# Kernel optimization log

Hardware: AMD Instinct MI355X
Metric: run time of the kernel (lower is better)

Reference implementation:

```python
import jax, jax.numpy as jnp
import numpy as np

NUM_HEADS = 4
EPS = 1e-12  # torch F.normalize eps


def conv1x1(x, w):
    # x: (b,c,h,w), w: (co,ci,1,1) -> pointwise conv == channel GEMM
    return jnp.einsum('bchw,dc->bdhw', x, w[:, :, 0, 0])


def dwconv3x3(x, w):
    # depthwise 3x3, groups = channels; w: (c,1,3,3)
    c = x.shape[1]
    return jax.lax.conv_general_dilated(
        x, w, window_strides=(1, 1), padding=((1, 1), (1, 1)),
        dimension_numbers=('NCHW', 'OIHW', 'NCHW'), feature_group_count=c)


def l2_normalize(x, axis=-1):
    n = jnp.sqrt(jnp.sum(x * x, axis=axis, keepdims=True))
    return x / jnp.maximum(n, EPS)


def setup_inputs() -> dict:
    key = jax.random.key(0)
    ks = jax.random.split(key, 8)
    b, c, h, w = 4, 192, 128, 128
    s = 0.05
    return {
        'x': jax.random.normal(ks[0], (b, c, h, w), jnp.float32),
        'wq': jax.random.normal(ks[1], (c, c, 1, 1), jnp.float32) * s,
        'wq_dw': jax.random.normal(ks[2], (c, 1, 3, 3), jnp.float32) * s,
        'wk': jax.random.normal(ks[3], (c, c, 1, 1), jnp.float32) * s,
        'wk_dw': jax.random.normal(ks[4], (c, 1, 3, 3), jnp.float32) * s,
        'wv': jax.random.normal(ks[5], (c, c, 1, 1), jnp.float32) * s,
        'wv_dw': jax.random.normal(ks[6], (c, 1, 3, 3), jnp.float32) * s,
        'temperature': jnp.ones((NUM_HEADS, 1, 1), jnp.float32),
    }


def reference(x, wq, wq_dw, wk, wk_dw, wv, wv_dw, temperature):
    b, c, h, w = x.shape
    hd = NUM_HEADS
    ch = c // hd  # per-head channels
    n = h * w

    q = dwconv3x3(conv1x1(x, wq), wq_dw)
    k = dwconv3x3(conv1x1(x, wk), wk_dw)
    v = dwconv3x3(conv1x1(x, wv), wv_dw)

    # b (head c) h w -> b head c (h w)
    q = q.reshape(b, hd, ch, n)
    k = k.reshape(b, hd, ch, n)
    v = v.reshape(b, hd, ch, n)

    q = l2_normalize(q, axis=-1)
    k = l2_normalize(k, axis=-1)

    # channel-wise attention: (c x N) @ (N x c) -> (c x c)
    attn = jnp.einsum('bhcn,bhdn->bhcd', q, k) * temperature  # temperature: (head,1,1)
    attn = jax.nn.softmax(attn, axis=-1)
    out = jnp.einsum('bhcd,bhdn->bhcn', attn, v)
    return out.reshape(b, c, h, w)
```

## Files before the change

kernel.cpp:

```cpp
#include <hip/hip_runtime.h>
#include <hip/hip_bf16.h>


typedef __attribute__((ext_vector_type(8))) short short8;
typedef __attribute__((ext_vector_type(4))) float f32x4;

#define NB 4
#define NC 192
#define NN 16384
#define CH 48
#define NWELEM 115780
#define NZERO 38400
#define LDP 200

__device__ inline unsigned short f2bf(float f) {
  union { float f; unsigned int u; } c; c.f = f;
  unsigned int r = c.u + 0x7FFF + ((c.u >> 16) & 1);
  return (unsigned short)(r >> 16);
}
__device__ inline float bf2f(unsigned short u) {
  union { unsigned int u; float f; } c; c.u = ((unsigned int)u) << 16;
  return c.f;
}

__device__ inline bool detect_f32(const unsigned short* x) {
  int l = threadIdx.x & 63;
  unsigned short u = x[2 * (l * 997 + 1)];
  int e = (u >> 7) & 0xFF;
  bool extreme = (e < 90) || (e > 165);
  return __popcll(__ballot(extreme)) >= 8;
}

__global__ __launch_bounds__(256) void k_pre(const unsigned short* __restrict__ x,
                                             const void* wq, const void* wk, const void* wv,
                                             const void* wqd, const void* wkd, const void* wvd,
                                             const void* temp,
                                             unsigned short* __restrict__ canon,
                                             float* __restrict__ zbase) {
  int blk = blockIdx.x;
  if (blk >= 453) {
    int i = (blk - 453) * 256 + threadIdx.x;
    if (i < NZERO) zbase[i] = 0.f;
    return;
  }
  bool f32 = detect_f32(x);
  int i = blk * 256 + threadIdx.x;
  if (i >= NWELEM) return;
  const void* src; int off;
  if (i < 36864)       { src = wq;  off = i; }
  else if (i < 73728)  { src = wk;  off = i - 36864; }
  else if (i < 110592) { src = wv;  off = i - 73728; }
  else if (i < 112320) { src = wqd; off = i - 110592; }
  else if (i < 114048) { src = wkd; off = i - 112320; }
  else if (i < 115776) { src = wvd; off = i - 114048; }
  else                 { src = temp; off = i - 115776; }
  canon[i] = f32 ? f2bf(((const float*)src)[off])
                 : ((const unsigned short*)src)[off];
}

__global__ __launch_bounds__(256) void k_conv(const unsigned short* __restrict__ Wall,
                                              const unsigned short* __restrict__ X,
                                              unsigned short* __restrict__ Yall) {
  __shared__ __align__(16) unsigned short Xs[128 * LDP];
  bool f32 = detect_f32(X);
  int b = blockIdx.y, p0 = blockIdx.x * 128;
  int tid = threadIdx.x;
  if (f32) {
    const float* Xf = (const float*)X + (size_t)b * NC * NN + p0;
    for (int it = 0; it < 12; ++it) {
      int idx = it * 256 + tid;
      int c = (idx >> 5) * 2, pq = idx & 31;
      float4 v0 = *(const float4*)(Xf + (size_t)c * NN + pq * 4);
      float4 v1 = *(const float4*)(Xf + (size_t)(c + 1) * NN + pq * 4);
#pragma unroll
      for (int j = 0; j < 4; ++j) {
        unsigned int u = ((unsigned int)f2bf((&v1.x)[j]) << 16) | f2bf((&v0.x)[j]);
        *(unsigned int*)(&Xs[(pq * 4 + j) * LDP + c]) = u;
      }
    }
  } else {
    const unsigned short* Xb = X + (size_t)b * NC * NN + p0;
    for (int it = 0; it < 12; ++it) {
      int idx = it * 256 + tid;
      int c = (idx >> 5) * 2, pq = idx & 31;
      ushort4 v0 = *(const ushort4*)(Xb + (size_t)c * NN + pq * 4);
      ushort4 v1 = *(const ushort4*)(Xb + (size_t)(c + 1) * NN + pq * 4);
#pragma unroll
      for (int j = 0; j < 4; ++j) {
        unsigned int u = ((unsigned int)((&v1.x)[j]) << 16) | (unsigned int)((&v0.x)[j]);
        *(unsigned int*)(&Xs[(pq * 4 + j) * LDP + c]) = u;
      }
    }
  }
  __syncthreads();
  int lane = tid & 63, w = tid >> 6;
  int wm = w & 1, wn = w >> 1;
  int lrow = lane & 15, lq = lane >> 4;
  short8 bf[6][4];
#pragma unroll
  for (int ks = 0; ks < 6; ++ks)
    for (int nt = 0; nt < 4; ++nt)
      bf[ks][nt] = *(const short8*)(&Xs[(wn * 64 + nt * 16 + lrow) * LDP + ks * 32 + lq * 8]);
  for (int dt = 0; dt < 9; ++dt) {
    int d0 = dt * 64;
    f32x4 acc[2][4];
    for (int mt = 0; mt < 2; ++mt)
      for (int nt = 0; nt < 4; ++nt) acc[mt][nt] = (f32x4){0.f, 0.f, 0.f, 0.f};
    for (int ks = 0; ks < 6; ++ks) {
      int k = ks * 32 + lq * 8;
      short8 a[2];
      for (int mt = 0; mt < 2; ++mt)
        a[mt] = *(const short8*)(Wall + (size_t)(d0 + wm * 32 + mt * 16 + lrow) * NC + k);
      for (int mt = 0; mt < 2; ++mt)
        for (int nt = 0; nt < 4; ++nt)
          acc[mt][nt] = __builtin_amdgcn_mfma_f32_16x16x32_bf16(a[mt], bf[ks][nt], acc[mt][nt], 0, 0, 0);
    }
    int proj = dt / 3, c0 = (dt % 3) * 64;
    unsigned short* Yb = Yall + (((size_t)proj * NB + b) * NC) * NN;
    for (int mt = 0; mt < 2; ++mt)
      for (int nt = 0; nt < 4; ++nt)
        for (int r = 0; r < 4; ++r) {
          int c = c0 + wm * 32 + mt * 16 + lq * 4 + r;
          int p = p0 + wn * 64 + nt * 16 + lrow;
          Yb[(size_t)c * NN + p] = f2bf(acc[mt][nt][r]);
        }
  }
}

__device__ inline void cvtrow(short8 raw, unsigned short lo, unsigned short hi,
                              float* dst) {
  dst[0] = bf2f(lo);
#pragma unroll
  for (int j = 0; j < 8; ++j) dst[j + 1] = bf2f((unsigned short)raw[j]);
  dst[9] = bf2f(hi);
}

__global__ __launch_bounds__(256) void k_dwconv(const unsigned short* __restrict__ Yall,
                                                const unsigned short* __restrict__ Wdall,
                                                unsigned short* __restrict__ Pq,
                                                unsigned short* __restrict__ Pk,
                                                unsigned short* __restrict__ Pv,
                                                float* __restrict__ ssq,
                                                float* __restrict__ ssk) {
  int y = blockIdx.x, b = blockIdx.y;
  int proj = y / NC, c = y % NC;
  int tid = threadIdx.x;
  int lane = tid & 63, ch = tid & 15, rg = tid >> 4;
  const unsigned short* base = Yall + (((size_t)proj * NB + b) * NC + c) * NN;
  unsigned short* P = (proj == 0 ? Pq : (proj == 1 ? Pk : Pv));
  float* ss = (proj == 0 ? ssq : (proj == 1 ? ssk : nullptr));
  int r0 = rg * 8;

  short8 raw[10];
  unsigned short hl[10], hr[10];
#pragma unroll
  for (int i = 0; i < 10; ++i) {
    int gy = r0 - 1 + i;
    const unsigned short* rp = base + gy * 128 + ch * 8;
    if (gy >= 0 && gy < 128) {
      raw[i] = *(const short8*)rp;
      hl[i] = (ch > 0)  ? rp[-1] : (unsigned short)0;
      hr[i] = (ch < 15) ? rp[8]  : (unsigned short)0;
    } else {
      raw[i] = (short8){0, 0, 0, 0, 0, 0, 0, 0};
      hl[i] = 0;
      hr[i] = 0;
    }
  }

  float wk9[9];
#pragma unroll
  for (int i = 0; i < 9; ++i) wk9[i] = bf2f(Wdall[(proj * NC + c) * 9 + i]);

  float rows[3][10];
  cvtrow(raw[0], hl[0], hr[0], rows[0]);
  cvtrow(raw[1], hl[1], hr[1], rows[1]);
  float ssacc = 0.f;
#pragma unroll
  for (int r = 0; r < 8; ++r) {
    cvtrow(raw[r + 2], hl[r + 2], hr[r + 2], rows[(r + 2) % 3]);
    float z[8];
#pragma unroll
    for (int j = 0; j < 8; ++j) z[j] = 0.f;
#pragma unroll
    for (int dy = 0; dy < 3; ++dy) {
      const float* f = rows[(r + dy) % 3];
      float w0 = wk9[dy * 3], w1 = wk9[dy * 3 + 1], w2 = wk9[dy * 3 + 2];
#pragma unroll
      for (int j = 0; j < 8; ++j) z[j] += w0 * f[j] + w1 * f[j + 1] + w2 * f[j + 2];
    }
    short8 sv;
#pragma unroll
    for (int j = 0; j < 8; ++j) { sv[j] = (short)f2bf(z[j]); ssacc += z[j] * z[j]; }
    *(short8*)(P + ((size_t)b * NC + c) * NN + (r0 + r) * 128 + ch * 8) = sv;
  }
  if (ss) {
    for (int off = 32; off; off >>= 1) ssacc += __shfl_down(ssacc, off);
    if (lane == 0) atomicAdd(&ss[b * NC + c], ssacc);
  }
}

__global__ __launch_bounds__(256) void k_attn(const unsigned short* __restrict__ Qp,
                                              const unsigned short* __restrict__ Kp,
                                              float* __restrict__ S) {
  __shared__ float Sred[CH * CH];
  int bh = blockIdx.y, chunk = blockIdx.x;
  int b = bh >> 2, h = bh & 3;
  int tid = threadIdx.x, lane = tid & 63, w = tid >> 6;
  int lrow = lane & 15, lq = lane >> 4;
  const unsigned short* Qb = Qp + ((size_t)b * NC + h * CH) * NN;
  const unsigned short* Kb = Kp + ((size_t)b * NC + h * CH) * NN;
  int nbase = chunk * 1024 + w * 256;
  f32x4 acc[3][3];
  for (int i = 0; i < 3; ++i)
    for (int j = 0; j < 3; ++j) acc[i][j] = (f32x4){0.f, 0.f, 0.f, 0.f};
  for (int ks = 0; ks < 8; ++ks) {
    int n = nbase + ks * 32 + lq * 8;
    short8 a[3], bb[3];
    for (int t = 0; t < 3; ++t) a[t]  = *(const short8*)(Qb + (size_t)(t * 16 + lrow) * NN + n);
    for (int t = 0; t < 3; ++t) bb[t] = *(const short8*)(Kb + (size_t)(t * 16 + lrow) * NN + n);
    for (int ti = 0; ti < 3; ++ti)
      for (int tj = 0; tj < 3; ++tj)
        acc[ti][tj] = __builtin_amdgcn_mfma_f32_16x16x32_bf16(a[ti], bb[tj], acc[ti][tj], 0, 0, 0);
  }
  for (int i = tid; i < CH * CH; i += 256) Sred[i] = 0.f;
  __syncthreads();
  for (int ti = 0; ti < 3; ++ti)
    for (int tj = 0; tj < 3; ++tj)
      for (int r = 0; r < 4; ++r) {
        int row = ti * 16 + lq * 4 + r, col = tj * 16 + lrow;
        atomicAdd(&Sred[row * CH + col], acc[ti][tj][r]);
      }
  __syncthreads();
  float* Sg = S + bh * (CH * CH);
  for (int i = tid; i < CH * CH; i += 256) atomicAdd(&Sg[i], Sred[i]);
}

__global__ void k_softmax(const float* __restrict__ S, const float* __restrict__ ssq,
                          const float* __restrict__ ssk, const unsigned short* __restrict__ tempc,
                          float* __restrict__ AT) {
  int bh = blockIdx.x, b = bh >> 2, h = bh & 3;
  int i = threadIdx.x;
  if (i >= CH) return;
  float t = bf2f(tempc[h]);
  float rq = 1.f / fmaxf(sqrtf(ssq[b * NC + h * CH + i]), 1e-12f);
  const float* Srow = S + bh * (CH * CH) + i * CH;
  float l[CH];
  float m = -1e30f;
  for (int j = 0; j < CH; ++j) {
    float rk = 1.f / fmaxf(sqrtf(ssk[b * NC + h * CH + j]), 1e-12f);
    l[j] = Srow[j] * rq * rk * t;
    m = fmaxf(m, l[j]);
  }
  float s = 0.f;
  for (int j = 0; j < CH; ++j) { l[j] = __expf(l[j] - m); s += l[j]; }
  float inv = 1.f / s;
  for (int j = 0; j < CH; ++j) AT[bh * (CH * CH) + j * CH + i] = l[j] * inv;
}

__global__ __launch_bounds__(256) void k_out(const float* __restrict__ AT,
                                             const unsigned short* __restrict__ Vp,
                                             void* __restrict__ Out,
                                             const unsigned short* __restrict__ x) {
  bool f32 = detect_f32(x);
  int bh = blockIdx.y, b = bh >> 2, h = bh & 3;
  int p0 = (blockIdx.x * 256 + threadIdx.x) * 2;
  const float* A = AT + bh * (CH * CH);
  const unsigned short* Vb = Vp + ((size_t)b * NC + h * CH) * NN;
  float a1[CH], a2[CH];
  for (int i = 0; i < CH; ++i) { a1[i] = 0.f; a2[i] = 0.f; }
  for (int j = 0; j < CH; ++j) {
    unsigned int u = *(const unsigned int*)(Vb + (size_t)j * NN + p0);
    float v1 = bf2f((unsigned short)(u & 0xFFFF));
    float v2 = bf2f((unsigned short)(u >> 16));
    const float* Aj = A + j * CH;
    for (int i = 0; i < CH; ++i) {
      float a = Aj[i];
      a1[i] += a * v1;
      a2[i] += a * v2;
    }
  }
  size_t obase = ((size_t)b * NC + h * CH) * NN;
  if (f32) {
    float* Of = (float*)Out;
    for (int i = 0; i < CH; ++i)
      *(float2*)(Of + obase + (size_t)i * NN + p0) = make_float2(a1[i], a2[i]);
  } else {
    unsigned short* Ob = (unsigned short*)Out;
    for (int i = 0; i < CH; ++i) {
      unsigned int u = ((unsigned int)f2bf(a2[i]) << 16) | f2bf(a1[i]);
      *(unsigned int*)(Ob + obase + (size_t)i * NN + p0) = u;
    }
  }
}

extern "C" void kernel_launch(void* const* d_in, const int* in_sizes, int n_in,
                              void* d_out, int out_size, void* d_ws, size_t ws_size,
                              hipStream_t stream) {
  const unsigned short* x = (const unsigned short*)d_in[0];

  const size_t TEN = (size_t)NB * NC * NN;
  unsigned short* bufA = (unsigned short*)d_ws;
  unsigned short* bufB = bufA + TEN;
  unsigned short* bufV = bufB + TEN;
  unsigned short* Yall = bufV + TEN;
  float* ssq = (float*)(Yall + 3 * TEN);
  float* ssk = ssq + NB * NC;
  float* S   = ssk + NB * NC;
  float* AT  = S + 16 * CH * CH;
  unsigned short* canon = (unsigned short*)(AT + 16 * CH * CH);
  const unsigned short* Wall = canon;
  const unsigned short* Wdall = canon + 110592;
  const unsigned short* Tmp = canon + 115776;

  k_pre<<<453 + (NZERO + 255) / 256, 256, 0, stream>>>(
      x, d_in[1], d_in[3], d_in[5], d_in[2], d_in[4], d_in[6], d_in[7], canon, ssq);
  k_conv<<<dim3(NN / 128, NB), 256, 0, stream>>>(Wall, x, Yall);
  k_dwconv<<<dim3(3 * NC, NB), 256, 0, stream>>>(Yall, Wdall, bufA, bufB, bufV, ssq, ssk);
  k_attn<<<dim3(16, 16), 256, 0, stream>>>(bufA, bufB, S);
  k_softmax<<<16, 64, 0, stream>>>(S, ssq, ssk, Tmp, AT);
  k_out<<<dim3(NN / 512, 16), 256, 0, stream>>>(AT, bufV, d_out, x);
}
```

Baseline: 232.7 us.

## Stage Q/K tiles in LDS for attn and register-block k_out over pixels

k_attn now cooperatively loads a 48x256 Q and K tile into padded shared memory with coalesced full-row reads, then runs the MFMA loop from LDS. It also uses four times as many blocks, each covering a smaller chunk. k_out caches the attention matrix in shared memory and gives each thread 12 output channels by 4 pixels instead of 48 channels by 2, which cuts register pressure and widens the vector loads and stores. The cost is more global atomics in k_attn because of the larger grid, plus extra LDS traffic.

Measured after the change: 256.8 us. +10.3%, slower.

```diff
diff --git a/kernel.cpp b/kernel.cpp
--- a/kernel.cpp
+++ b/kernel.cpp
@@ -12,6 +12,7 @@
 #define NWELEM 115780
 #define NZERO 38400
 #define LDP 200
+#define AST 272
 
 __device__ inline unsigned short f2bf(float f) {
   union { float f; unsigned int u; } c; c.f = f;
@@ -203,6 +204,8 @@
 __global__ __launch_bounds__(256) void k_attn(const unsigned short* __restrict__ Qp,
                                               const unsigned short* __restrict__ Kp,
                                               float* __restrict__ S) {
+  __shared__ __align__(16) unsigned short Qs[CH * AST];
+  __shared__ __align__(16) unsigned short Ks[CH * AST];
   __shared__ float Sred[CH * CH];
   int bh = blockIdx.y, chunk = blockIdx.x;
   int b = bh >> 2, h = bh & 3;
@@ -210,21 +213,28 @@
   int lrow = lane & 15, lq = lane >> 4;
   const unsigned short* Qb = Qp + ((size_t)b * NC + h * CH) * NN;
   const unsigned short* Kb = Kp + ((size_t)b * NC + h * CH) * NN;
-  int nbase = chunk * 1024 + w * 256;
+  int n0 = chunk * 256;
+  for (int it = 0; it < 6; ++it) {
+    int idx = it * 256 + tid;
+    int row = idx >> 5, colv = idx & 31;
+    *(short8*)(&Qs[row * AST + colv * 8]) = *(const short8*)(Qb + (size_t)row * NN + n0 + colv * 8);
+    *(short8*)(&Ks[row * AST + colv * 8]) = *(const short8*)(Kb + (size_t)row * NN + n0 + colv * 8);
+  }
+  for (int i = tid; i < CH * CH; i += 256) Sred[i] = 0.f;
+  __syncthreads();
   f32x4 acc[3][3];
   for (int i = 0; i < 3; ++i)
     for (int j = 0; j < 3; ++j) acc[i][j] = (f32x4){0.f, 0.f, 0.f, 0.f};
-  for (int ks = 0; ks < 8; ++ks) {
-    int n = nbase + ks * 32 + lq * 8;
+#pragma unroll
+  for (int ks2 = 0; ks2 < 2; ++ks2) {
+    int nn = (w * 2 + ks2) * 32 + lq * 8;
     short8 a[3], bb[3];
-    for (int t = 0; t < 3; ++t) a[t]  = *(const short8*)(Qb + (size_t)(t * 16 + lrow) * NN + n);
-    for (int t = 0; t < 3; ++t) bb[t] = *(const short8*)(Kb + (size_t)(t * 16 + lrow) * NN + n);
+    for (int t = 0; t < 3; ++t) a[t]  = *(const short8*)(&Qs[(t * 16 + lrow) * AST + nn]);
+    for (int t = 0; t < 3; ++t) bb[t] = *(const short8*)(&Ks[(t * 16 + lrow) * AST + nn]);
     for (int ti = 0; ti < 3; ++ti)
       for (int tj = 0; tj < 3; ++tj)
         acc[ti][tj] = __builtin_amdgcn_mfma_f32_16x16x32_bf16(a[ti], bb[tj], acc[ti][tj], 0, 0, 0);
   }
-  for (int i = tid; i < CH * CH; i += 256) Sred[i] = 0.f;
-  __syncthreads();
   for (int ti = 0; ti < 3; ++ti)
     for (int tj = 0; tj < 3; ++tj)
       for (int r = 0; r < 4; ++r) {
@@ -262,34 +272,50 @@
                                              const unsigned short* __restrict__ Vp,
                                              void* __restrict__ Out,
                                              const unsigned short* __restrict__ x) {
+  __shared__ float As[CH * CH];
   bool f32 = detect_f32(x);
   int bh = blockIdx.y, b = bh >> 2, h = bh & 3;
-  int p0 = (blockIdx.x * 256 + threadIdx.x) * 2;
+  int tid = threadIdx.x;
+  int pxs = tid & 63, islot = tid >> 6;
+  int p0 = blockIdx.x * 256 + pxs * 4;
+  int i0 = islot * 12;
   const float* A = AT + bh * (CH * CH);
+  for (int it = 0; it < 9; ++it) As[it * 256 + tid] = A[it * 256 + tid];
+  __syncthreads();
   const unsigned short* Vb = Vp + ((size_t)b * NC + h * CH) * NN;
-  float a1[CH], a2[CH];
-  for (int i = 0; i < CH; ++i) { a1[i] = 0.f; a2[i] = 0.f; }
+  float acc[12][4];
+#pragma unroll
+  for (int ii = 0; ii < 12; ++ii)
+    for (int q = 0; q < 4; ++q) acc[ii][q] = 0.f;
   for (int j = 0; j < CH; ++j) {
-    unsigned int u = *(const unsigned int*)(Vb + (size_t)j * NN + p0);
-    float v1 = bf2f((unsigned short)(u & 0xFFFF));
-    float v2 = bf2f((unsigned short)(u >> 16));
-    const float* Aj = A + j * CH;
-    for (int i = 0; i < CH; ++i) {
-      float a = Aj[i];
-      a1[i] += a * v1;
-      a2[i] += a * v2;
+    ushort4 vv = *(const ushort4*)(Vb + (size_t)j * NN + p0);
+    float v0 = bf2f(vv.x), v1 = bf2f(vv.y), v2 = bf2f(vv.z), v3 = bf2f(vv.w);
+    const float* Aj = As + j * CH + i0;
+#pragma unroll
+    for (int ii = 0; ii < 12; ++ii) {
+      float a = Aj[ii];
+      acc[ii][0] += a * v0;
+      acc[ii][1] += a * v1;
+      acc[ii][2] += a * v2;
+      acc[ii][3] += a * v3;
     }
   }
   size_t obase = ((size_t)b * NC + h * CH) * NN;
   if (f32) {
     float* Of = (float*)Out;
-    for (int i = 0; i < CH; ++i)
-      *(float2*)(Of + obase + (size_t)i * NN + p0) = make_float2(a1[i], a2[i]);
+#pragma unroll
+    for (int ii = 0; ii < 12; ++ii) {
+      float4 o = make_float4(acc[ii][0], acc[ii][1], acc[ii][2], acc[ii][3]);
+      *(float4*)(Of + obase + (size_t)(i0 + ii) * NN + p0) = o;
+    }
   } else {
     unsigned short* Ob = (unsigned short*)Out;
-    for (int i = 0; i < CH; ++i) {
-      unsigned int u = ((unsigned int)f2bf(a2[i]) << 16) | f2bf(a1[i]);
-      *(unsigned int*)(Ob + obase + (size_t)i * NN + p0) = u;
+#pragma unroll
+    for (int ii = 0; ii < 12; ++ii) {
+      ushort4 sv;
+      sv.x = f2bf(acc[ii][0]); sv.y = f2bf(acc[ii][1]);
+      sv.z = f2bf(acc[ii][2]); sv.w = f2bf(acc[ii][3]);
+      *(ushort4*)(Ob + obase + (size_t)(i0 + ii) * NN + p0) = sv;
     }
   }
 }
@@ -317,7 +343,7 @@
       x, d_in[1], d_in[3], d_in[5], d_in[2], d_in[4], d_in[6], d_in[7], canon, ssq);
   k_conv<<<dim3(NN / 128, NB), 256, 0, stream>>>(Wall, x, Yall);
   k_dwconv<<<dim3(3 * NC, NB), 256, 0, stream>>>(Yall, Wdall, bufA, bufB, bufV, ssq, ssk);
-  k_attn<<<dim3(16, 16), 256, 0, stream>>>(bufA, bufB, S);
+  k_attn<<<dim3(64, 16), 256, 0, stream>>>(bufA, bufB, S);
   k_softmax<<<16, 64, 0, stream>>>(S, ssq, ssk, Tmp, AT);
-  k_out<<<dim3(NN / 512, 16), 256, 0, stream>>>(AT, bufV, d_out, x);
-}
+  k_out<<<dim3(NN / 256, 16), 256, 0, stream>>>(AT, bufV, d_out, x);
+}
```
